# Kernel tuning notes

Hardware: AMD Instinct MI355X
Metric: run time of the kernel (lower is better)

Reference implementation:

```python
import jax, jax.numpy as jnp
import numpy as np

N = 50000
E = 800000
IN_C = 128
HID = 128
NUM_CLASSES = 64


def setup_inputs() -> dict:
    key = jax.random.key(0)
    ks = jax.random.split(key, 8)
    x = jax.random.normal(ks[0], (N, IN_C), dtype=jnp.float32)
    edge_index = jax.random.randint(ks[1], (2, E), 0, N, dtype=jnp.int64)
    # Xavier-uniform style weights stored as [in, out]; biases zero-init.
    def xavier(k, fan_in, fan_out):
        lim = float(np.sqrt(6.0 / (fan_in + fan_out)))
        return jax.random.uniform(k, (fan_in, fan_out), minval=-lim, maxval=lim, dtype=jnp.float32)
    W1 = xavier(ks[2], IN_C, HID)
    b1 = jnp.zeros((HID,), dtype=jnp.float32)
    W2 = xavier(ks[3], HID, HID)
    b2 = jnp.zeros((HID,), dtype=jnp.float32)
    W3 = xavier(ks[4], HID, NUM_CLASSES)
    b3 = jnp.zeros((NUM_CLASSES,), dtype=jnp.float32)
    return {"x": x, "edge_index": edge_index, "W1": W1, "b1": b1, "W2": W2, "b2": b2, "W3": W3, "b3": b3}


def _add_self_loops(edge_index, num_nodes):
    loops = jnp.arange(num_nodes, dtype=edge_index.dtype)
    row = jnp.concatenate([edge_index[0], loops])
    col = jnp.concatenate([edge_index[1], loops])
    return row, col


def _gcn_layer(x, row, col, dinv, W, b):
    # x: [N, Cin] -> h: [N, Cout]; symmetric-normalized scatter-add aggregation.
    h = x @ W
    norm = dinv[row] * dinv[col]              # [E']
    msg = norm[:, None] * h[row]              # gather + scale (dropout is a no-op in eval)
    out = jax.ops.segment_sum(msg, col, num_segments=x.shape[0])
    return out + b


def reference(x, edge_index, W1, b1, W2, b2, W3, b3):
    n = x.shape[0]
    row, col = _add_self_loops(edge_index, n)
    deg = jax.ops.segment_sum(jnp.ones_like(col, dtype=x.dtype), col, num_segments=n)
    dinv = jnp.where(deg > 0, deg ** -0.5, 0.0)
    h1 = jax.nn.relu(_gcn_layer(x, row, col, dinv, W1, b1))
    h2 = jax.nn.relu(_gcn_layer(h1, row, col, dinv, W2, b2))
    out = _gcn_layer(h2, row, col, dinv, W3, b3)
    return (h2, out)
```

## Files before the change

kernel.cpp:

```cpp
#include <hip/hip_runtime.h>
#include <hip/hip_bf16.h>


typedef float vf4 __attribute__((ext_vector_type(4)));
typedef unsigned vu4 __attribute__((ext_vector_type(4)));
typedef unsigned vu2 __attribute__((ext_vector_type(2)));
typedef short bf8v __attribute__((ext_vector_type(8)));
typedef float f4v __attribute__((ext_vector_type(4)));

__device__ __forceinline__ float bits2f(unsigned u) {
    union { unsigned u; float f; } c; c.u = u; return c.f;
}
__device__ __forceinline__ unsigned short f2bfu(float v) {
    __hip_bfloat16 h = __float2bfloat16(v);
    union { __hip_bfloat16 h; unsigned short u; } c; c.h = h; return c.u;
}
__device__ __forceinline__ float bflo(unsigned d) { return bits2f(d << 16); }
__device__ __forceinline__ float bfhi(unsigned d) { return bits2f(d & 0xffff0000u); }

__global__ void detect_dtypes(const void* __restrict__ x,
                              const void* __restrict__ ei,
                              int* __restrict__ flags) {
    const int t = threadIdx.x;
    const int lane = t & 63;
    if (t < 64) {
        const unsigned short* p = (const unsigned short*)x;
        int e = (p[2 * (lane * 16)] >> 7) & 0xFF;
        unsigned long long m = __ballot(e < 100 || e > 140);
        if (lane == 0) flags[0] = (__popcll(m) > 16) ? 1 : 0;
    } else if (t < 128) {
        const int* p = (const int*)ei;
        unsigned long long m = __ballot(p[2 * (lane * 16) + 1] != 0);
        if (lane == 0) flags[1] = (__popcll(m) < 2) ? 1 : 0;
    }
}

__device__ __forceinline__ int edge_at(const void* ei, long long idx, bool i64) {
    return i64 ? (int)((const long long*)ei)[idx] : ((const int*)ei)[idx];
}

__global__ void convert_count(const void* __restrict__ ei,
                              int* __restrict__ row32, int* __restrict__ col32,
                              int* __restrict__ rank32,
                              int* __restrict__ cnt,
                              const int* __restrict__ flags, int e) {
    int i = blockIdx.x * 256 + threadIdx.x;
    if (i < e) {
        const bool i64 = flags[1] != 0;
        int r = edge_at(ei, i, i64);
        int c = edge_at(ei, (long long)e + i, i64);
        row32[i] = r;
        col32[i] = c;
        rank32[i] = atomicAdd(&cnt[c], 1);
    }
}

__global__ __launch_bounds__(256) void deg_reduce(const int* __restrict__ cnt,
                                                  int* __restrict__ bsum, int n) {
    __shared__ int sm[4];
    const int t = threadIdx.x;
    int i = blockIdx.x * 256 + t;
    int v = (i < n) ? cnt[i] : 0;
#pragma unroll
    for (int d = 32; d >= 1; d >>= 1) v += __shfl_down(v, d);
    if ((t & 63) == 0) sm[t >> 6] = v;
    __syncthreads();
    if (t == 0) bsum[blockIdx.x] = sm[0] + sm[1] + sm[2] + sm[3];
}

__global__ __launch_bounds__(256) void scan_bsums(int* __restrict__ bsum, int nb) {
    __shared__ int sm[256];
    const int t = threadIdx.x;
    sm[t] = (t < nb) ? bsum[t] : 0;
    __syncthreads();
#pragma unroll
    for (int d = 1; d < 256; d <<= 1) {
        int v = (t >= d) ? sm[t - d] : 0;
        __syncthreads();
        sm[t] += v;
        __syncthreads();
    }
    if (t < nb) bsum[t] = (t == 0) ? 0 : sm[t - 1];
}

__global__ __launch_bounds__(256) void write_off(const int* __restrict__ cnt,
                                                 const int* __restrict__ bsum,
                                                 int* __restrict__ off,
                                                 float* __restrict__ dinv,
                                                 int n, int e_total) {
    __shared__ int sm[256];
    const int t = threadIdx.x;
    const int i = blockIdx.x * 256 + t;
    const int c = (i < n) ? cnt[i] : 0;
    sm[t] = c;
    __syncthreads();
#pragma unroll
    for (int d = 1; d < 256; d <<= 1) {
        int v = (t >= d) ? sm[t - d] : 0;
        __syncthreads();
        sm[t] += v;
        __syncthreads();
    }
    if (i < n) {
        int o = bsum[blockIdx.x] + sm[t] - c;
        off[i] = o;
        dinv[i] = rsqrtf((float)(c + 1));
        if (i == n - 1) off[n] = e_total;
    }
}

__global__ void fill_csr(const int* __restrict__ row32, const int* __restrict__ col32,
                         const int* __restrict__ rank32, const int* __restrict__ off,
                         int* __restrict__ csr_src, int e) {
    int i = blockIdx.x * 256 + threadIdx.x;
    if (i < e) {
        csr_src[off[col32[i]] + rank32[i]] = row32[i];
    }
}

template <int COUT, bool XDYN>
__global__ __launch_bounds__(256) void gemm_mfma(const void* __restrict__ Xv,
                                                 const void* __restrict__ Wv,
                                                 const float* __restrict__ dinv,
                                                 unsigned short* __restrict__ G,
                                                 const int* __restrict__ flags, int n) {
    constexpr int WS = 132;
    __shared__ __align__(16) short Wt[COUT * WS];
    const int t = threadIdx.x;
    const bool f32 = flags[0] != 0;

    if (f32) {
        const float* W = (const float*)Wv;
        for (int i = t; i < 128 * COUT; i += 256) {
            int k = i / COUT, c = i % COUT;
            Wt[c * WS + k] = (short)f2bfu(W[i]);
        }
    } else {
        const short* W = (const short*)Wv;
        for (int i = t; i < 128 * COUT; i += 256) {
            int k = i / COUT, c = i % COUT;
            Wt[c * WS + k] = W[i];
        }
    }
    __syncthreads();

    const int w = t >> 6, l = t & 63;
    const int m = l & 15, q = l >> 4;
    const int row = blockIdx.x * 64 + w * 16 + m;
    const int xrow = min(row, n - 1);

    bf8v xf[4];
    if (XDYN && f32) {
        const float* X = (const float*)Xv;
#pragma unroll
        for (int ks = 0; ks < 4; ++ks) {
            const float4 a = *(const float4*)&X[(size_t)xrow * 128 + ks * 32 + q * 8];
            const float4 b = *(const float4*)&X[(size_t)xrow * 128 + ks * 32 + q * 8 + 4];
            bf8v v;
            v[0] = (short)f2bfu(a.x); v[1] = (short)f2bfu(a.y);
            v[2] = (short)f2bfu(a.z); v[3] = (short)f2bfu(a.w);
            v[4] = (short)f2bfu(b.x); v[5] = (short)f2bfu(b.y);
            v[6] = (short)f2bfu(b.z); v[7] = (short)f2bfu(b.w);
            xf[ks] = v;
        }
    } else {
        const short* X = (const short*)Xv;
#pragma unroll
        for (int ks = 0; ks < 4; ++ks)
            xf[ks] = *(const bf8v*)&X[(size_t)xrow * 128 + ks * 32 + q * 8];
    }
    const float dv = dinv[xrow];

#pragma unroll
    for (int ct = 0; ct < COUT / 16; ++ct) {
        f4v acc = {0.f, 0.f, 0.f, 0.f};
#pragma unroll
        for (int ks = 0; ks < 4; ++ks) {
            bf8v wf = *(const bf8v*)&Wt[(ct * 16 + m) * WS + ks * 32 + q * 8];
            acc = __builtin_amdgcn_mfma_f32_16x16x32_bf16(wf, xf[ks], acc, 0, 0, 0);
        }
        if (row < n) {
            vu2 u;
            u.x = (unsigned)f2bfu(dv * acc[0]) | ((unsigned)f2bfu(dv * acc[1]) << 16);
            u.y = (unsigned)f2bfu(dv * acc[2]) | ((unsigned)f2bfu(dv * acc[3]) << 16);
            *(vu2*)&G[(size_t)row * COUT + ct * 16 + q * 4] = u;
        }
    }
}

template <int CPL, bool RELU, bool WWS, bool WOUT>
__global__ __launch_bounds__(256) void aggregate(const unsigned* __restrict__ Gd,
                                                 const int* __restrict__ off,
                                                 const int* __restrict__ csr_src,
                                                 const float* __restrict__ dinv,
                                                 const void* __restrict__ bias,
                                                 unsigned* __restrict__ Hws,
                                                 void* __restrict__ outp,
                                                 long long out_off,
                                                 const int* __restrict__ flags, int n) {
    const int gw = (int)((blockIdx.x * 256u + threadIdx.x) >> 6);
    const int lane = threadIdx.x & 63;
    if (gw >= n) return;
    constexpr int C = CPL * 64;
    constexpr int LPG = (CPL == 2) ? 16 : 8;
    constexpr int GROUPS = 64 / LPG;
    constexpr int RD = C / 2;
    const int g = lane / LPG;
    const int li = lane % LPG;
    const int e0 = off[gw];
    const int e1 = off[gw + 1];
    const float d = dinv[gw];

    float acc[8];
    {
        uint4 sv = *(const uint4*)&Gd[(size_t)gw * RD + li * 4];
        const float ms = (g == 0) ? 1.f : 0.f;
        acc[0] = ms * bflo(sv.x); acc[1] = ms * bfhi(sv.x);
        acc[2] = ms * bflo(sv.y); acc[3] = ms * bfhi(sv.y);
        acc[4] = ms * bflo(sv.z); acc[5] = ms * bfhi(sv.z);
        acc[6] = ms * bflo(sv.w); acc[7] = ms * bfhi(sv.w);
    }

    for (int bs = e0; bs < e1; bs += 64) {
        const int cnt = min(64, e1 - bs);
        const int myidx = (bs + lane < e1) ? csr_src[bs + lane] : 0;
        for (int j = 0; j < cnt; j += 2 * GROUPS) {
#pragma unroll
            for (int u = 0; u < 2; ++u) {
                const int eb = j + u * GROUPS + g;
                const int jj = min(eb, cnt - 1);
                const int s = __shfl(myidx, jj);
                const float m = (eb < cnt) ? 1.f : 0.f;
                uint4 v = *(const uint4*)&Gd[(size_t)s * RD + li * 4];
                acc[0] = fmaf(m, bflo(v.x), acc[0]);
                acc[1] = fmaf(m, bfhi(v.x), acc[1]);
                acc[2] = fmaf(m, bflo(v.y), acc[2]);
                acc[3] = fmaf(m, bfhi(v.y), acc[3]);
                acc[4] = fmaf(m, bflo(v.z), acc[4]);
                acc[5] = fmaf(m, bfhi(v.z), acc[5]);
                acc[6] = fmaf(m, bflo(v.w), acc[6]);
                acc[7] = fmaf(m, bfhi(v.w), acc[7]);
            }
        }
    }

#pragma unroll
    for (int mask = LPG; mask <= 32; mask <<= 1)
#pragma unroll
        for (int i = 0; i < 8; ++i) acc[i] += __shfl_xor(acc[i], mask);

    const bool f32 = flags[0] != 0;
    float bvf[8];
    if (f32) {
        const float* B = (const float*)bias;
        const float4 b0 = *(const float4*)&B[li * 8];
        const float4 b1 = *(const float4*)&B[li * 8 + 4];
        bvf[0] = b0.x; bvf[1] = b0.y; bvf[2] = b0.z; bvf[3] = b0.w;
        bvf[4] = b1.x; bvf[5] = b1.y; bvf[6] = b1.z; bvf[7] = b1.w;
    } else {
        const uint4 bv = *(const uint4*)&((const unsigned*)bias)[li * 4];
        bvf[0] = bflo(bv.x); bvf[1] = bfhi(bv.x);
        bvf[2] = bflo(bv.y); bvf[3] = bfhi(bv.y);
        bvf[4] = bflo(bv.z); bvf[5] = bfhi(bv.z);
        bvf[6] = bflo(bv.w); bvf[7] = bfhi(bv.w);
    }
    float o[8];
#pragma unroll
    for (int i = 0; i < 8; ++i) {
        o[i] = d * acc[i] + bvf[i];
        if (RELU) o[i] = fmaxf(o[i], 0.f);
    }

    if (g == 0) {
        if constexpr (WWS) {
            vu4 u;
            u.x = (unsigned)f2bfu(o[0]) | ((unsigned)f2bfu(o[1]) << 16);
            u.y = (unsigned)f2bfu(o[2]) | ((unsigned)f2bfu(o[3]) << 16);
            u.z = (unsigned)f2bfu(o[4]) | ((unsigned)f2bfu(o[5]) << 16);
            u.w = (unsigned)f2bfu(o[6]) | ((unsigned)f2bfu(o[7]) << 16);
            unsigned* hb = Hws + (size_t)gw * RD + li * 4;
            __builtin_nontemporal_store(u, (vu4*)hb);
        }
        if constexpr (WOUT) {
            if (f32) {
                float* po = (float*)outp + out_off + (size_t)gw * C + li * 8;
                vf4 w0 = {o[0], o[1], o[2], o[3]};
                vf4 w1 = {o[4], o[5], o[6], o[7]};
                __builtin_nontemporal_store(w0, (vf4*)po);
                __builtin_nontemporal_store(w1, (vf4*)po + 1);
            } else {
                vu4 u;
                u.x = (unsigned)f2bfu(o[0]) | ((unsigned)f2bfu(o[1]) << 16);
                u.y = (unsigned)f2bfu(o[2]) | ((unsigned)f2bfu(o[3]) << 16);
                u.z = (unsigned)f2bfu(o[4]) | ((unsigned)f2bfu(o[5]) << 16);
                u.w = (unsigned)f2bfu(o[6]) | ((unsigned)f2bfu(o[7]) << 16);
                unsigned* ob = (unsigned*)outp + (out_off >> 1) + (size_t)gw * RD + li * 4;
                __builtin_nontemporal_store(u, (vu4*)ob);
            }
        }
    }
}

extern "C" void kernel_launch(void* const* d_in, const int* in_sizes, int n_in,
                              void* d_out, int out_size, void* d_ws, size_t ws_size,
                              hipStream_t stream) {
    const void* x  = d_in[0];
    const void* ei = d_in[1];
    const void* W1 = d_in[2];
    const void* b1 = d_in[3];
    const void* W2 = d_in[4];
    const void* b2 = d_in[5];
    const void* W3 = d_in[6];
    const void* b3 = d_in[7];

    const int N = in_sizes[0] / 128;
    const int E = in_sizes[1] / 2;

    char* p = (char*)d_ws;
    auto take = [&](size_t bytes) {
        char* q = p;
        p += (bytes + 255) & ~(size_t)255;
        return q;
    };
    int*   flags   = (int*)take(64);
    int*   cnt     = (int*)take((size_t)N * 4);
    int*   bsum    = (int*)take(1024);
    int*   off     = (int*)take((size_t)(N + 1) * 4);
    float* dinv    = (float*)take((size_t)N * 4);
    int*   row32   = (int*)take((size_t)E * 4);
    int*   col32   = (int*)take((size_t)E * 4);
    int*   rank32  = (int*)take((size_t)E * 4);
    int*   csr     = (int*)take((size_t)E * 4);
    unsigned short* bufA = (unsigned short*)take((size_t)N * 128 * 2);
    unsigned short* bufB = (unsigned short*)take((size_t)N * 128 * 2);
    (void)n_in; (void)out_size; (void)ws_size;

    const int nb = (N + 255) / 256;
    const int eb = (E + 255) / 256;

    detect_dtypes<<<1, 128, 0, stream>>>(x, ei, flags);
    hipMemsetAsync(cnt, 0, (size_t)N * 4, stream);
    convert_count<<<eb, 256, 0, stream>>>(ei, row32, col32, rank32, cnt, flags, E);
    deg_reduce<<<nb, 256, 0, stream>>>(cnt, bsum, N);
    scan_bsums<<<1, 256, 0, stream>>>(bsum, nb);
    write_off<<<nb, 256, 0, stream>>>(cnt, bsum, off, dinv, N, E);
    fill_csr<<<eb, 256, 0, stream>>>(row32, col32, rank32, off, csr, E);

    const int gb = (N + 63) / 64;
    const int ab = (N + 3) / 4;

    gemm_mfma<128, true><<<gb, 256, 0, stream>>>(x, W1, dinv, bufA, flags, N);
    aggregate<2, true, true, false><<<ab, 256, 0, stream>>>((const unsigned*)bufA, off, csr, dinv, b1, (unsigned*)bufB, nullptr, 0, flags, N);
    gemm_mfma<128, false><<<gb, 256, 0, stream>>>(bufB, W2, dinv, bufA, flags, N);
    aggregate<2, true, true, true><<<ab, 256, 0, stream>>>((const unsigned*)bufA, off, csr, dinv, b2, (unsigned*)bufB, d_out, 0, flags, N);
    gemm_mfma<64, false><<<gb, 256, 0, stream>>>(bufB, W3, dinv, bufA, flags, N);
    aggregate<1, false, false, true><<<ab, 256, 0, stream>>>((const unsigned*)bufA, off, csr, dinv, b3, nullptr, d_out, (long long)N * 128, flags, N);
}
```

Baseline: 272.5 us.

## Build CSR via per-block LDS histograms instead of global atomics

Replaces the global-atomic degree count and rank computation with a three-step scheme. Each of 256 blocks builds a packed 16-bit-pair histogram of destination nodes in shared memory. A column scan then produces per-block offsets, and a scatter pass reassigns ranks with LDS atomics. This removes contended global atomics and the rank32 array, but adds a 256×25000 histogram written to and read back from global memory. It depends on N fitting in 100KB of LDS and on per-node counts staying below 65536.

```diff
diff --git a/kernel.cpp b/kernel.cpp
--- a/kernel.cpp
+++ b/kernel.cpp
@@ -7,6 +7,9 @@
 typedef unsigned vu2 __attribute__((ext_vector_type(2)));
 typedef short bf8v __attribute__((ext_vector_type(8)));
 typedef float f4v __attribute__((ext_vector_type(4)));
+
+constexpr int PCAP = 25000;
+constexpr int NHB  = 256;
 
 __device__ __forceinline__ float bits2f(unsigned u) {
     union { unsigned u; float f; } c; c.u = u; return c.f;
@@ -37,6 +40,80 @@
 
 __device__ __forceinline__ int edge_at(const void* ei, long long idx, bool i64) {
     return i64 ? (int)((const long long*)ei)[idx] : ((const int*)ei)[idx];
+}
+
+__global__ __launch_bounds__(1024) void hist_count(const void* __restrict__ ei,
+                                                   int* __restrict__ row32,
+                                                   int* __restrict__ col32,
+                                                   unsigned* __restrict__ histg,
+                                                   const int* __restrict__ flags,
+                                                   int e, int epb, int pc) {
+    __shared__ unsigned h[PCAP];
+    const int t = threadIdx.x;
+    const int b = blockIdx.x;
+    for (int j = t; j < pc; j += 1024) h[j] = 0u;
+    __syncthreads();
+    const bool i64 = flags[1] != 0;
+    const int base = b * epb;
+    const int end = min(e, base + epb);
+    for (int i = base + t; i < end; i += 1024) {
+        int r = edge_at(ei, i, i64);
+        int c = edge_at(ei, (long long)e + i, i64);
+        row32[i] = r;
+        col32[i] = c;
+        atomicAdd(&h[c >> 1], (c & 1) ? 0x10000u : 1u);
+    }
+    __syncthreads();
+    unsigned* out = histg + (size_t)b * pc;
+    for (int j = t; j < pc; j += 1024) out[j] = h[j];
+}
+
+__global__ __launch_bounds__(256) void hist_scan(unsigned* __restrict__ histg,
+                                                 int* __restrict__ cnt, int pc, int n) {
+    __shared__ unsigned tile[NHB][65];
+    const int t = threadIdx.x;
+    const int c = t & 63;
+    const int jc = blockIdx.x * 64 + c;
+    for (int r = t >> 6; r < NHB; r += 4)
+        tile[r][c] = (jc < pc) ? histg[(size_t)r * pc + jc] : 0u;
+    __syncthreads();
+    if (t < 64 && jc < pc) {
+        unsigned run = 0;
+        for (int r = 0; r < NHB; ++r) {
+            unsigned v = tile[r][t];
+            tile[r][t] = run;
+            run += v;
+        }
+        int c0 = jc * 2;
+        if (c0 < n) cnt[c0] = (int)(run & 0xffffu);
+        if (c0 + 1 < n) cnt[c0 + 1] = (int)(run >> 16);
+    }
+    __syncthreads();
+    for (int r = t >> 6; r < NHB; r += 4)
+        if (jc < pc) histg[(size_t)r * pc + jc] = tile[r][c];
+}
+
+__global__ __launch_bounds__(1024) void scatter_fill(const int* __restrict__ row32,
+                                                     const int* __restrict__ col32,
+                                                     const unsigned* __restrict__ histg,
+                                                     const int* __restrict__ off,
+                                                     int* __restrict__ csr,
+                                                     int e, int epb, int pc) {
+    __shared__ unsigned h[PCAP];
+    const int t = threadIdx.x;
+    const int b = blockIdx.x;
+    const unsigned* src = histg + (size_t)b * pc;
+    for (int j = t; j < pc; j += 1024) h[j] = src[j];
+    __syncthreads();
+    const int base = b * epb;
+    const int end = min(e, base + epb);
+    for (int i = base + t; i < end; i += 1024) {
+        int r = row32[i];
+        int c = col32[i];
+        unsigned old = atomicAdd(&h[c >> 1], (c & 1) ? 0x10000u : 1u);
+        unsigned rank = (c & 1) ? (old >> 16) : (old & 0xffffu);
+        csr[off[c] + (int)rank] = r;
+    }
 }
 
 __global__ void convert_count(const void* __restrict__ ei,
@@ -55,6 +132,15 @@
     }
 }
 
+__global__ void fill_csr(const int* __restrict__ row32, const int* __restrict__ col32,
+                         const int* __restrict__ rank32, const int* __restrict__ off,
+                         int* __restrict__ csr_src, int e) {
+    int i = blockIdx.x * 256 + threadIdx.x;
+    if (i < e) {
+        csr_src[off[col32[i]] + rank32[i]] = row32[i];
+    }
+}
+
 __global__ __launch_bounds__(256) void deg_reduce(const int* __restrict__ cnt,
                                                   int* __restrict__ bsum, int n) {
     __shared__ int sm[4];
@@ -106,15 +192,6 @@
         off[i] = o;
         dinv[i] = rsqrtf((float)(c + 1));
         if (i == n - 1) off[n] = e_total;
-    }
-}
-
-__global__ void fill_csr(const int* __restrict__ row32, const int* __restrict__ col32,
-                         const int* __restrict__ rank32, const int* __restrict__ off,
-                         int* __restrict__ csr_src, int e) {
-    int i = blockIdx.x * 256 + threadIdx.x;
-    if (i < e) {
-        csr_src[off[col32[i]] + rank32[i]] = row32[i];
     }
 }
 
@@ -322,15 +399,17 @@
         p += (bytes + 255) & ~(size_t)255;
         return q;
     };
-    int*   flags   = (int*)take(64);
-    int*   cnt     = (int*)take((size_t)N * 4);
-    int*   bsum    = (int*)take(1024);
-    int*   off     = (int*)take((size_t)(N + 1) * 4);
-    float* dinv    = (float*)take((size_t)N * 4);
-    int*   row32   = (int*)take((size_t)E * 4);
-    int*   col32   = (int*)take((size_t)E * 4);
-    int*   rank32  = (int*)take((size_t)E * 4);
-    int*   csr     = (int*)take((size_t)E * 4);
+    int*      flags = (int*)take(64);
+    int*      cnt   = (int*)take((size_t)N * 4);
+    int*      bsum  = (int*)take(1024);
+    int*      off   = (int*)take((size_t)(N + 1) * 4);
+    float*    dinv  = (float*)take((size_t)N * 4);
+    int*      row32 = (int*)take((size_t)E * 4);
+    int*      col32 = (int*)take((size_t)E * 4);
+    int*      csr   = (int*)take((size_t)E * 4);
+    const int pc    = (N + 1) / 2;
+    unsigned* histg = (unsigned*)take((size_t)NHB * (size_t)((pc <= PCAP) ? pc : 0) * 4);
+    int*      rank32 = (int*)take((pc <= PCAP) ? 0 : (size_t)E * 4);
     unsigned short* bufA = (unsigned short*)take((size_t)N * 128 * 2);
     unsigned short* bufB = (unsigned short*)take((size_t)N * 128 * 2);
     (void)n_in; (void)out_size; (void)ws_size;
@@ -339,12 +418,23 @@
     const int eb = (E + 255) / 256;
 
     detect_dtypes<<<1, 128, 0, stream>>>(x, ei, flags);
-    hipMemsetAsync(cnt, 0, (size_t)N * 4, stream);
-    convert_count<<<eb, 256, 0, stream>>>(ei, row32, col32, rank32, cnt, flags, E);
-    deg_reduce<<<nb, 256, 0, stream>>>(cnt, bsum, N);
-    scan_bsums<<<1, 256, 0, stream>>>(bsum, nb);
-    write_off<<<nb, 256, 0, stream>>>(cnt, bsum, off, dinv, N, E);
-    fill_csr<<<eb, 256, 0, stream>>>(row32, col32, rank32, off, csr, E);
+
+    if (pc <= PCAP) {
+        const int epb = (E + NHB - 1) / NHB;
+        hist_count<<<NHB, 1024, 0, stream>>>(ei, row32, col32, histg, flags, E, epb, pc);
+        hist_scan<<<(pc + 63) / 64, 256, 0, stream>>>(histg, cnt, pc, N);
+        deg_reduce<<<nb, 256, 0, stream>>>(cnt, bsum, N);
+        scan_bsums<<<1, 256, 0, stream>>>(bsum, nb);
+        write_off<<<nb, 256, 0, stream>>>(cnt, bsum, off, dinv, N, E);
+        scatter_fill<<<NHB, 1024, 0, stream>>>(row32, col32, histg, off, csr, E, epb, pc);
+    } else {
+        hipMemsetAsync(cnt, 0, (size_t)N * 4, stream);
+        convert_count<<<eb, 256, 0, stream>>>(ei, row32, col32, rank32, cnt, flags, E);
+        deg_reduce<<<nb, 256, 0, stream>>>(cnt, bsum, N);
+        scan_bsums<<<1, 256, 0, stream>>>(bsum, nb);
+        write_off<<<nb, 256, 0, stream>>>(cnt, bsum, off, dinv, N, E);
+        fill_csr<<<eb, 256, 0, stream>>>(row32, col32, rank32, off, csr, E);
+    }
 
     const int gb = (N + 63) / 64;
     const int ab = (N + 3) / 4;
```

Result: no change. 271.3 us (-0.5%).
